# Kernel optimization log

Hardware: AMD Instinct MI355X
Metric: run time of the kernel (lower is better)

Reference implementation:

```python
import jax, jax.numpy as jnp
import numpy as np


def setup_inputs() -> dict:
    key = jax.random.key(0)
    ks = jax.random.split(key, 7)
    N, T, E = 4, 2048, 1024
    s = 1.0 / np.sqrt(E)
    return {
        "X": jax.random.normal(ks[0], (N, T, E), dtype=jnp.float32),
        "Wq": jax.random.normal(ks[1], (E, E), dtype=jnp.float32) * s,
        "bq": jax.random.normal(ks[2], (E,), dtype=jnp.float32) * 0.01,
        "Wk": jax.random.normal(ks[3], (E, E), dtype=jnp.float32) * s,
        "bk": jax.random.normal(ks[4], (E,), dtype=jnp.float32) * 0.01,
        "Wv": jax.random.normal(ks[5], (E, E), dtype=jnp.float32) * s,
        "bv": jax.random.normal(ks[6], (E,), dtype=jnp.float32) * 0.01,
    }


def reference(X, Wq, bq, Wk, bk, Wv, bv):
    # QKV projections: [N,T,E] @ [E,E] + [E]
    q = jnp.einsum("nte,ef->ntf", X, Wq) + bq
    k = jnp.einsum("nte,ef->ntf", X, Wk) + bk
    v = jnp.einsum("nte,ef->ntf", X, Wv) + bv
    # Unscaled full attention (module does NOT divide by sqrt(E))
    sim = jnp.einsum("nqe,nke->nqk", q, k)         # [N,T,T]
    weight = jax.nn.softmax(sim, axis=2)
    return jnp.einsum("nqk,nke->nqe", weight, v)    # [N,T,E]
```

## Files before the change

kernel.cpp:

```cpp
#include <hip/hip_runtime.h>

typedef unsigned short u16;
typedef unsigned int u32;
typedef float floatx4 __attribute__((ext_vector_type(4)));
typedef __bf16 bf16x8 __attribute__((ext_vector_type(8)));

__device__ __forceinline__ u16 bf16_rne(float x) {
  u32 u = __builtin_bit_cast(u32, x);
  return (u16)((u + 0x7FFFu + ((u >> 16) & 1u)) >> 16);
}
__device__ __forceinline__ float bf16f(u16 h) {
  u32 u = ((u32)h) << 16;
  return __builtin_bit_cast(float, u);
}
__device__ __forceinline__ void g2l16(const u16* g, u16* l) {
  __builtin_amdgcn_global_load_lds((const __attribute__((address_space(1))) u32*)g,
                                   (__attribute__((address_space(3))) u32*)l, 16, 0, 0);
}
__device__ __forceinline__ floatx4 mfma16(bf16x8 a, bf16x8 b, floatx4 c) {
  return __builtin_amdgcn_mfma_f32_16x16x32_bf16(a, b, c, 0, 0, 0);
}
#define SB() __builtin_amdgcn_sched_barrier(0)

__device__ __forceinline__ void xcd_swizzle(int& bx, int& by, int& bz) {
  const int gx = gridDim.x, gy = gridDim.y;
  int nb = gx * gy * gridDim.z;
  int flat = blockIdx.x + gx * (blockIdx.y + gy * blockIdx.z);
  int swz = flat;
  if ((nb & 7) == 0) {
    int cpx = nb >> 3;
    swz = (flat & 7) * cpx + (flat >> 3);
  }
  bz = swz / (gx * gy);
  int rem = swz - bz * gx * gy;
  by = rem / gx;
  bx = rem - by * gx;
}

__global__ void split_x_kernel(const float* __restrict__ X, u16* __restrict__ Xh,
                               u16* __restrict__ Xl, int n4) {
  int i = blockIdx.x * blockDim.x + threadIdx.x;
  int stride = gridDim.x * blockDim.x;
  for (; i < n4; i += stride) {
    float4 x = reinterpret_cast<const float4*>(X)[i];
    float v[4] = {x.x, x.y, x.z, x.w};
    u16 hh[4], ll[4];
#pragma unroll
    for (int j = 0; j < 4; ++j) {
      hh[j] = bf16_rne(v[j]);
      ll[j] = bf16_rne(v[j] - bf16f(hh[j]));
    }
    reinterpret_cast<ushort4*>(Xh)[i] = make_ushort4(hh[0], hh[1], hh[2], hh[3]);
    reinterpret_cast<ushort4*>(Xl)[i] = make_ushort4(ll[0], ll[1], ll[2], ll[3]);
  }
}

__global__ void wsplit_t_kernel(const float* __restrict__ W, u16* __restrict__ Th,
                                u16* __restrict__ Tl) {
  __shared__ float tile[32][33];
  int tx = threadIdx.x, ty = threadIdx.y;
  int f0 = blockIdx.x * 32, e0 = blockIdx.y * 32;
  tile[ty][tx] = W[(e0 + ty) * 1024 + f0 + tx];
  __syncthreads();
  float v = tile[tx][ty];
  u16 h = bf16_rne(v);
  Th[(f0 + ty) * 1024 + e0 + tx] = h;
  Tl[(f0 + ty) * 1024 + e0 + tx] = bf16_rne(v - bf16f(h));
}

template <int EPI>
__global__ __launch_bounds__(512, 2) void gemm8_split(
    const u16* __restrict__ Ah, const u16* __restrict__ Al,
    const u16* __restrict__ Bh, const u16* __restrict__ Bl,
    float* __restrict__ C, u16* __restrict__ Oh, u16* __restrict__ Ol,
    const float* __restrict__ b1, const float* __restrict__ b2, int NH,
    int N, int K, int lda, int ldb, long sA, long sB, long sC) {
  __shared__ u16 lds[2][4][256 * 32];
  const int tid = threadIdx.x;
  int bx, by, bz;
  xcd_swizzle(bx, by, bz);
  const int z = bz;
  const int brow = by * 256;
  const int bcol = bx * 256;
  const int w = tid >> 6, l = tid & 63;
  const int wm = w >> 2, wn = w & 3;
  const int fr = l & 15, kq = l >> 4;

  const u16* gA0 = Ah + (long)z * sA + (long)brow * lda;
  const u16* gA1 = Al + (long)z * sA + (long)brow * lda;
  const u16* gB0 = Bh + (long)z * sB + (long)bcol * ldb;
  const u16* gB1 = Bl + (long)z * sB + (long)bcol * ldb;

  const int r0 = tid >> 2, s0 = tid & 3;
  const int r1 = (tid + 512) >> 2, s1 = (tid + 512) & 3;
  const long aOff0 = (long)r0 * lda + ((s0 ^ ((r0 >> 1) & 3)) << 3);
  const long aOff1 = (long)r1 * lda + ((s1 ^ ((r1 >> 1) & 3)) << 3);
  const long bOff0 = (long)r0 * ldb + ((s0 ^ ((r0 >> 1) & 3)) << 3);
  const long bOff1 = (long)r1 * ldb + ((s1 ^ ((r1 >> 1) & 3)) << 3);
  const int d0 = tid * 8, d1 = (tid + 512) * 8;

  auto STAGE = [&](int b, int k0) {
    g2l16(gA0 + aOff0 + k0, &lds[b][0][d0]);
    g2l16(gA0 + aOff1 + k0, &lds[b][0][d1]);
    g2l16(gA1 + aOff0 + k0, &lds[b][1][d0]);
    g2l16(gA1 + aOff1 + k0, &lds[b][1][d1]);
    g2l16(gB0 + bOff0 + k0, &lds[b][2][d0]);
    g2l16(gB0 + bOff1 + k0, &lds[b][2][d1]);
    g2l16(gB1 + bOff0 + k0, &lds[b][3][d0]);
    g2l16(gB1 + bOff1 + k0, &lds[b][3][d1]);
  };

  int aoffs[8], boffs[4];
#pragma unroll
  for (int m = 0; m < 8; ++m) {
    int r = wm * 128 + m * 16 + fr;
    aoffs[m] = r * 32 + (((kq ^ (r >> 1)) & 3) << 3);
  }
#pragma unroll
  for (int n = 0; n < 4; ++n) {
    int r = wn * 64 + n * 16 + fr;
    boffs[n] = r * 32 + (((kq ^ (r >> 1)) & 3) << 3);
  }

  floatx4 acc[8][4];
#pragma unroll
  for (int m = 0; m < 8; ++m)
#pragma unroll
    for (int n = 0; n < 4; ++n)
#pragma unroll
      for (int j = 0; j < 4; ++j) acc[m][n][j] = 0.f;

  const int NT = K >> 5;
  STAGE(0, 0);
  STAGE(1, 32);
  SB();
  asm volatile("s_waitcnt vmcnt(8)" ::: "memory");
  SB(); __builtin_amdgcn_s_barrier(); SB();

  bf16x8 fa_h[4], fa_l[4], fb_h[4], fb_l[4];

  for (int t = 0; t < NT; ++t) {
    const int p = t & 1;
    const u16* LAh = &lds[p][0][0];
    const u16* LAl = &lds[p][1][0];
    const u16* LBh = &lds[p][2][0];
    const u16* LBl = &lds[p][3][0];

#pragma unroll
    for (int m = 0; m < 4; ++m) {
      fa_h[m] = *(const bf16x8*)(LAh + aoffs[m]);
      fa_l[m] = *(const bf16x8*)(LAl + aoffs[m]);
    }
#pragma unroll
    for (int n = 0; n < 2; ++n) {
      fb_h[n] = *(const bf16x8*)(LBh + boffs[n]);
      fb_l[n] = *(const bf16x8*)(LBl + boffs[n]);
    }
    SB(); __builtin_amdgcn_s_barrier();
    asm volatile("s_waitcnt lgkmcnt(0)" ::: "memory");
    SB();
    __builtin_amdgcn_s_setprio(1);
#pragma unroll
    for (int m = 0; m < 4; ++m)
#pragma unroll
      for (int n = 0; n < 2; ++n) acc[m][n] = mfma16(fa_h[m], fb_h[n], acc[m][n]);
#pragma unroll
    for (int m = 0; m < 4; ++m)
#pragma unroll
      for (int n = 0; n < 2; ++n) acc[m][n] = mfma16(fa_h[m], fb_l[n], acc[m][n]);
#pragma unroll
    for (int m = 0; m < 4; ++m)
#pragma unroll
      for (int n = 0; n < 2; ++n) acc[m][n] = mfma16(fa_l[m], fb_h[n], acc[m][n]);
    __builtin_amdgcn_s_setprio(0);
    SB(); __builtin_amdgcn_s_barrier(); SB();

#pragma unroll
    for (int n = 2; n < 4; ++n) {
      fb_h[n] = *(const bf16x8*)(LBh + boffs[n]);
      fb_l[n] = *(const bf16x8*)(LBl + boffs[n]);
    }
    SB(); __builtin_amdgcn_s_barrier();
    asm volatile("s_waitcnt lgkmcnt(0)" ::: "memory");
    SB();
    __builtin_amdgcn_s_setprio(1);
#pragma unroll
    for (int m = 0; m < 4; ++m)
#pragma unroll
      for (int n = 2; n < 4; ++n) acc[m][n] = mfma16(fa_h[m], fb_h[n], acc[m][n]);
#pragma unroll
    for (int m = 0; m < 4; ++m)
#pragma unroll
      for (int n = 2; n < 4; ++n) acc[m][n] = mfma16(fa_h[m], fb_l[n], acc[m][n]);
#pragma unroll
    for (int m = 0; m < 4; ++m)
#pragma unroll
      for (int n = 2; n < 4; ++n) acc[m][n] = mfma16(fa_l[m], fb_h[n], acc[m][n]);
    __builtin_amdgcn_s_setprio(0);
    SB(); __builtin_amdgcn_s_barrier(); SB();

#pragma unroll
    for (int m = 0; m < 4; ++m) {
      fa_h[m] = *(const bf16x8*)(LAh + aoffs[m + 4]);
      fa_l[m] = *(const bf16x8*)(LAl + aoffs[m + 4]);
    }
    SB(); __builtin_amdgcn_s_barrier();
    asm volatile("s_waitcnt lgkmcnt(0)" ::: "memory");
    SB();
    __builtin_amdgcn_s_setprio(1);
#pragma unroll
    for (int m = 0; m < 4; ++m)
#pragma unroll
      for (int n = 0; n < 2; ++n) acc[m + 4][n] = mfma16(fa_h[m], fb_h[n], acc[m + 4][n]);
#pragma unroll
    for (int m = 0; m < 4; ++m)
#pragma unroll
      for (int n = 0; n < 2; ++n) acc[m + 4][n] = mfma16(fa_h[m], fb_l[n], acc[m + 4][n]);
#pragma unroll
    for (int m = 0; m < 4; ++m)
#pragma unroll
      for (int n = 0; n < 2; ++n) acc[m + 4][n] = mfma16(fa_l[m], fb_h[n], acc[m + 4][n]);
    __builtin_amdgcn_s_setprio(0);
    SB(); __builtin_amdgcn_s_barrier(); SB();

    if (t + 2 < NT) STAGE(p, (t + 2) << 5);
    SB();
    __builtin_amdgcn_s_setprio(1);
#pragma unroll
    for (int m = 0; m < 4; ++m)
#pragma unroll
      for (int n = 2; n < 4; ++n) acc[m + 4][n] = mfma16(fa_h[m], fb_h[n], acc[m + 4][n]);
#pragma unroll
    for (int m = 0; m < 4; ++m)
#pragma unroll
      for (int n = 2; n < 4; ++n) acc[m + 4][n] = mfma16(fa_h[m], fb_l[n], acc[m + 4][n]);
#pragma unroll
    for (int m = 0; m < 4; ++m)
#pragma unroll
      for (int n = 2; n < 4; ++n) acc[m + 4][n] = mfma16(fa_l[m], fb_h[n], acc[m + 4][n]);
    __builtin_amdgcn_s_setprio(0);
    SB();
    if (t + 2 < NT) {
      asm volatile("s_waitcnt vmcnt(8)" ::: "memory");
    } else {
      asm volatile("s_waitcnt vmcnt(0)" ::: "memory");
    }
    SB(); __builtin_amdgcn_s_barrier(); SB();
  }

#pragma unroll
  for (int m = 0; m < 8; ++m)
#pragma unroll
    for (int n = 0; n < 4; ++n)
#pragma unroll
      for (int j = 0; j < 4; ++j) {
        int gr = brow + wm * 128 + m * 16 + kq * 4 + j;
        int gc = bcol + wn * 64 + n * 16 + fr;
        float v = acc[m][n][j];
        if (EPI == 0) {
          C[(long)z * sC + (long)gr * N + gc] = v;
        } else {
          v += (gc < NH) ? b1[gc] : b2[gc - NH];
          u16 h = bf16_rne(v);
          long idx = (long)gr * N + gc;
          Oh[idx] = h;
          Ol[idx] = bf16_rne(v - bf16f(h));
        }
      }
}

template <int EPI>
__global__ __launch_bounds__(512, 2) void gemm8_plain(
    const u16* __restrict__ A, const u16* __restrict__ B,
    float* __restrict__ C, u16* __restrict__ Oh, const float* __restrict__ bias,
    int N, int K, int lda, int ldb, long sA, long sB, long sC) {
  __shared__ u16 lds[2][24576];
  const int BOFF = 8192;
  const int tid = threadIdx.x;
  int bx, by, bz;
  xcd_swizzle(bx, by, bz);
  const int z = bz;
  const int brow = by * 128;
  const int bcol = bx * 256;
  const int w = tid >> 6, l = tid & 63;
  const int wm = (w >> 2) * 64, wn = (w & 3) * 64;
  const int fr = l & 15, kq = l >> 4;

  const u16* gA = A + (long)z * sA + (long)brow * lda;
  const u16* gB = B + (long)z * sB + (long)bcol * ldb;

  long aO[2], bO[4];
  int aD[2], bD[4];
#pragma unroll
  for (int i = 0; i < 2; ++i) {
    int c = tid + i * 512, r = c >> 3, s = c & 7;
    aO[i] = (long)r * lda + ((s ^ (r & 7)) << 3);
    aD[i] = c * 8;
  }
#pragma unroll
  for (int i = 0; i < 4; ++i) {
    int c = tid + i * 512, r = c >> 3, s = c & 7;
    bO[i] = (long)r * ldb + ((s ^ (r & 7)) << 3);
    bD[i] = BOFF + c * 8;
  }

  auto STAGE = [&](int b, int k0) {
#pragma unroll
    for (int i = 0; i < 2; ++i) g2l16(gA + aO[i] + k0, &lds[b][aD[i]]);
#pragma unroll
    for (int i = 0; i < 4; ++i) g2l16(gB + bO[i] + k0, &lds[b][bD[i]]);
  };

  int aoffs[4][2], boffs[4][2];
#pragma unroll
  for (int m = 0; m < 4; ++m) {
    int r = wm + m * 16 + fr;
#pragma unroll
    for (int k = 0; k < 2; ++k) aoffs[m][k] = r * 64 + ((((k * 4 + kq) ^ r) & 7) << 3);
  }
#pragma unroll
  for (int n = 0; n < 4; ++n) {
    int r = wn + n * 16 + fr;
#pragma unroll
    for (int k = 0; k < 2; ++k) boffs[n][k] = BOFF + r * 64 + ((((k * 4 + kq) ^ r) & 7) << 3);
  }

  floatx4 acc[4][4];
#pragma unroll
  for (int m = 0; m < 4; ++m)
#pragma unroll
    for (int n = 0; n < 4; ++n)
#pragma unroll
      for (int j = 0; j < 4; ++j) acc[m][n][j] = 0.f;

  const int NT = K >> 6;
  STAGE(0, 0);
  STAGE(1, 64);
  SB();
  asm volatile("s_waitcnt vmcnt(6)" ::: "memory");
  SB(); __builtin_amdgcn_s_barrier(); SB();

  bf16x8 fa[2][2], fb[4][2];

  for (int t = 0; t < NT; ++t) {
    const int p = t & 1;
    const u16* L = &lds[p][0];

#pragma unroll
    for (int m = 0; m < 2; ++m)
#pragma unroll
      for (int k = 0; k < 2; ++k) fa[m][k] = *(const bf16x8*)(L + aoffs[m][k]);
#pragma unroll
    for (int n = 0; n < 2; ++n)
#pragma unroll
      for (int k = 0; k < 2; ++k) fb[n][k] = *(const bf16x8*)(L + boffs[n][k]);
    SB(); __builtin_amdgcn_s_barrier();
    asm volatile("s_waitcnt lgkmcnt(0)" ::: "memory");
    SB();
    __builtin_amdgcn_s_setprio(1);
#pragma unroll
    for (int m = 0; m < 2; ++m)
#pragma unroll
      for (int n = 0; n < 2; ++n) acc[m][n] = mfma16(fa[m][0], fb[n][0], acc[m][n]);
#pragma unroll
    for (int m = 0; m < 2; ++m)
#pragma unroll
      for (int n = 0; n < 2; ++n) acc[m][n] = mfma16(fa[m][1], fb[n][1], acc[m][n]);
    __builtin_amdgcn_s_setprio(0);
    SB(); __builtin_amdgcn_s_barrier(); SB();

#pragma unroll
    for (int n = 2; n < 4; ++n)
#pragma unroll
      for (int k = 0; k < 2; ++k) fb[n][k] = *(const bf16x8*)(L + boffs[n][k]);
    SB(); __builtin_amdgcn_s_barrier();
    asm volatile("s_waitcnt lgkmcnt(0)" ::: "memory");
    SB();
    __builtin_amdgcn_s_setprio(1);
#pragma unroll
    for (int m = 0; m < 2; ++m)
#pragma unroll
      for (int n = 2; n < 4; ++n) acc[m][n] = mfma16(fa[m][0], fb[n][0], acc[m][n]);
#pragma unroll
    for (int m = 0; m < 2; ++m)
#pragma unroll
      for (int n = 2; n < 4; ++n) acc[m][n] = mfma16(fa[m][1], fb[n][1], acc[m][n]);
    __builtin_amdgcn_s_setprio(0);
    SB(); __builtin_amdgcn_s_barrier(); SB();

#pragma unroll
    for (int m = 0; m < 2; ++m)
#pragma unroll
      for (int k = 0; k < 2; ++k) fa[m][k] = *(const bf16x8*)(L + aoffs[m + 2][k]);
    SB(); __builtin_amdgcn_s_barrier();
    asm volatile("s_waitcnt lgkmcnt(0)" ::: "memory");
    SB();
    __builtin_amdgcn_s_setprio(1);
#pragma unroll
    for (int m = 0; m < 2; ++m)
#pragma unroll
      for (int n = 0; n < 2; ++n) acc[m + 2][n] = mfma16(fa[m][0], fb[n][0], acc[m + 2][n]);
#pragma unroll
    for (int m = 0; m < 2; ++m)
#pragma unroll
      for (int n = 0; n < 2; ++n) acc[m + 2][n] = mfma16(fa[m][1], fb[n][1], acc[m + 2][n]);
    __builtin_amdgcn_s_setprio(0);
    SB(); __builtin_amdgcn_s_barrier(); SB();

    if (t + 2 < NT) STAGE(p, (t + 2) << 6);
    SB();
    __builtin_amdgcn_s_setprio(1);
#pragma unroll
    for (int m = 0; m < 2; ++m)
#pragma unroll
      for (int n = 2; n < 4; ++n) acc[m + 2][n] = mfma16(fa[m][0], fb[n][0], acc[m + 2][n]);
#pragma unroll
    for (int m = 0; m < 2; ++m)
#pragma unroll
      for (int n = 2; n < 4; ++n) acc[m + 2][n] = mfma16(fa[m][1], fb[n][1], acc[m + 2][n]);
    __builtin_amdgcn_s_setprio(0);
    SB();
    if (t + 2 < NT) {
      asm volatile("s_waitcnt vmcnt(6)" ::: "memory");
    } else {
      asm volatile("s_waitcnt vmcnt(0)" ::: "memory");
    }
    SB(); __builtin_amdgcn_s_barrier(); SB();
  }

#pragma unroll
  for (int m = 0; m < 4; ++m)
#pragma unroll
    for (int n = 0; n < 4; ++n)
#pragma unroll
      for (int j = 0; j < 4; ++j) {
        int gr = brow + wm + m * 16 + kq * 4 + j;
        int gc = bcol + wn + n * 16 + fr;
        float v = acc[m][n][j];
        if (EPI == 0) {
          C[(long)z * sC + (long)gr * N + gc] = v;
        } else {
          v += bias[gc];
          long oi = ((long)((gr >> 11) * 1024 + gc)) * 2048 + (gr & 2047);
          Oh[oi] = bf16_rne(v);
        }
      }
}

__global__ __launch_bounds__(256) void softmax_kernel(const float* __restrict__ S,
                                                      u16* __restrict__ Wgt) {
  const long row = blockIdx.x;
  const float4* src = reinterpret_cast<const float4*>(S + row * 2048);
  const int t = threadIdx.x;
  float4 x0 = src[t];
  float4 x1 = src[t + 256];
  float m = fmaxf(fmaxf(fmaxf(x0.x, x0.y), fmaxf(x0.z, x0.w)),
                  fmaxf(fmaxf(x1.x, x1.y), fmaxf(x1.z, x1.w)));
#pragma unroll
  for (int s = 32; s > 0; s >>= 1) m = fmaxf(m, __shfl_xor(m, s));
  __shared__ float redm[4];
  __shared__ float reds[4];
  if ((t & 63) == 0) redm[t >> 6] = m;
  __syncthreads();
  m = fmaxf(fmaxf(redm[0], redm[1]), fmaxf(redm[2], redm[3]));
  float e[8];
  e[0] = __expf(x0.x - m); e[1] = __expf(x0.y - m);
  e[2] = __expf(x0.z - m); e[3] = __expf(x0.w - m);
  e[4] = __expf(x1.x - m); e[5] = __expf(x1.y - m);
  e[6] = __expf(x1.z - m); e[7] = __expf(x1.w - m);
  float s = ((e[0] + e[1]) + (e[2] + e[3])) + ((e[4] + e[5]) + (e[6] + e[7]));
#pragma unroll
  for (int k = 32; k > 0; k >>= 1) s += __shfl_xor(s, k);
  if ((t & 63) == 0) reds[t >> 6] = s;
  __syncthreads();
  s = (reds[0] + reds[1]) + (reds[2] + reds[3]);
  float inv = 1.f / s;
  u32* dst = reinterpret_cast<u32*>(Wgt + row * 2048);
  dst[2 * t] = (u32)bf16_rne(e[0] * inv) | ((u32)bf16_rne(e[1] * inv) << 16);
  dst[2 * t + 1] = (u32)bf16_rne(e[2] * inv) | ((u32)bf16_rne(e[3] * inv) << 16);
  dst[2 * (t + 256)] = (u32)bf16_rne(e[4] * inv) | ((u32)bf16_rne(e[5] * inv) << 16);
  dst[2 * (t + 256) + 1] = (u32)bf16_rne(e[6] * inv) | ((u32)bf16_rne(e[7] * inv) << 16);
}

extern "C" void kernel_launch(void* const* d_in, const int* in_sizes, int n_in,
                              void* d_out, int out_size, void* d_ws, size_t ws_size,
                              hipStream_t stream) {
  const float* X = (const float*)d_in[0];
  const float* Wq = (const float*)d_in[1];
  const float* bq = (const float*)d_in[2];
  const float* Wk = (const float*)d_in[3];
  const float* bk = (const float*)d_in[4];
  const float* Wv = (const float*)d_in[5];
  const float* bv = (const float*)d_in[6];
  float* out = (float*)d_out;

  char* ws = (char*)d_ws;
  const size_t MB = 1ull << 20;
  u16* Xh = (u16*)(ws + 0 * MB);
  u16* Xl = (u16*)(ws + 16 * MB);
  u16* Wqkh = (u16*)(ws + 32 * MB);
  u16* Wqkl = (u16*)(ws + 36 * MB);
  u16* Wvh = (u16*)(ws + 40 * MB);
  u16* Wvl = (u16*)(ws + 42 * MB);
  float* sim = (float*)(ws);
  u16* qkh = (u16*)(ws + 64 * MB);
  u16* qkl = (u16*)(ws + 96 * MB);
  u16* vt = (u16*)(ws + 128 * MB);
  u16* wb = (u16*)(ws + 64 * MB);

  split_x_kernel<<<4096, 256, 0, stream>>>(X, Xh, Xl, (8192 * 1024) / 4);
  wsplit_t_kernel<<<dim3(32, 32), dim3(32, 32), 0, stream>>>(Wq, Wqkh, Wqkl);
  wsplit_t_kernel<<<dim3(32, 32), dim3(32, 32), 0, stream>>>(Wk, Wqkh + 1024 * 1024,
                                                             Wqkl + 1024 * 1024);
  wsplit_t_kernel<<<dim3(32, 32), dim3(32, 32), 0, stream>>>(Wv, Wvh, Wvl);
  gemm8_split<1><<<dim3(8, 32, 1), 512, 0, stream>>>(
      Xh, Xl, Wqkh, Wqkl, nullptr, qkh, qkl, bq, bk, 1024,
      2048, 1024, 1024, 1024, 0, 0, 0);
  gemm8_plain<2><<<dim3(4, 64, 1), 512, 0, stream>>>(
      Xh, Wvh, nullptr, vt, bv, 1024, 1024, 1024, 1024, 0, 0, 0);
  gemm8_split<0><<<dim3(8, 8, 4), 512, 0, stream>>>(
      qkh, qkl, qkh + 1024, qkl + 1024, sim, nullptr, nullptr, nullptr, nullptr, 0,
      2048, 1024, 2048, 2048, 2048L * 2048, 2048L * 2048, 2048L * 2048);
  softmax_kernel<<<8192, 256, 0, stream>>>(sim, wb);
  gemm8_plain<0><<<dim3(4, 16, 4), 512, 0, stream>>>(
      wb, vt, out, nullptr, nullptr, 1024, 2048, 2048, 2048,
      2048L * 2048, 1024L * 2048, 2048L * 1024);
}
```

Measured before the change: 357.2 us.

## Switch GEMM kernels from 16x16x32 to 32x32x16 MFMA tiles

Replaces the 16x16x32 bf16 MFMA instruction with the 32x32x16 variant in both GEMM kernels. The LDS fragment offsets, accumulator layout and epilogue index mapping are reworked to match, and the per-iteration schedule shrinks from four sub-phases with barriers to two k-substeps. The larger MFMA tile needs fewer LDS fragment reads per FLOP and fewer barriers, at the cost of different register pressure and less interleaving of loads with compute.

```diff
diff --git a/kernel.cpp b/kernel.cpp
--- a/kernel.cpp
+++ b/kernel.cpp
@@ -2,7 +2,7 @@
 
 typedef unsigned short u16;
 typedef unsigned int u32;
-typedef float floatx4 __attribute__((ext_vector_type(4)));
+typedef float floatx16 __attribute__((ext_vector_type(16)));
 typedef __bf16 bf16x8 __attribute__((ext_vector_type(8)));
 
 __device__ __forceinline__ u16 bf16_rne(float x) {
@@ -17,8 +17,8 @@
   __builtin_amdgcn_global_load_lds((const __attribute__((address_space(1))) u32*)g,
                                    (__attribute__((address_space(3))) u32*)l, 16, 0, 0);
 }
-__device__ __forceinline__ floatx4 mfma16(bf16x8 a, bf16x8 b, floatx4 c) {
-  return __builtin_amdgcn_mfma_f32_16x16x32_bf16(a, b, c, 0, 0, 0);
+__device__ __forceinline__ floatx16 mfma32(bf16x8 a, bf16x8 b, floatx16 c) {
+  return __builtin_amdgcn_mfma_f32_32x32x16_bf16(a, b, c, 0, 0, 0);
 }
 #define SB() __builtin_amdgcn_sched_barrier(0)
 
@@ -84,7 +84,7 @@
   const int bcol = bx * 256;
   const int w = tid >> 6, l = tid & 63;
   const int wm = w >> 2, wn = w & 3;
-  const int fr = l & 15, kq = l >> 4;
+  const int lr = l & 31, lh = l >> 5;
 
   const u16* gA0 = Ah + (long)z * sA + (long)brow * lda;
   const u16* gA1 = Al + (long)z * sA + (long)brow * lda;
@@ -110,25 +110,29 @@
     g2l16(gB1 + bOff1 + k0, &lds[b][3][d1]);
   };
 
-  int aoffs[8], boffs[4];
-#pragma unroll
-  for (int m = 0; m < 8; ++m) {
-    int r = wm * 128 + m * 16 + fr;
-    aoffs[m] = r * 32 + (((kq ^ (r >> 1)) & 3) << 3);
-  }
-#pragma unroll
-  for (int n = 0; n < 4; ++n) {
-    int r = wn * 64 + n * 16 + fr;
-    boffs[n] = r * 32 + (((kq ^ (r >> 1)) & 3) << 3);
-  }
-
-  floatx4 acc[8][4];
-#pragma unroll
-  for (int m = 0; m < 8; ++m)
-#pragma unroll
-    for (int n = 0; n < 4; ++n)
-#pragma unroll
-      for (int j = 0; j < 4; ++j) acc[m][n][j] = 0.f;
+  int aoffs[4][2], boffs[2][2];
+#pragma unroll
+  for (int m = 0; m < 4; ++m) {
+    int r = wm * 128 + m * 32 + lr;
+#pragma unroll
+    for (int ks = 0; ks < 2; ++ks)
+      aoffs[m][ks] = r * 32 + ((((ks * 2 + lh) ^ ((r >> 1) & 3)) & 3) << 3);
+  }
+#pragma unroll
+  for (int n = 0; n < 2; ++n) {
+    int r = wn * 64 + n * 32 + lr;
+#pragma unroll
+    for (int ks = 0; ks < 2; ++ks)
+      boffs[n][ks] = r * 32 + ((((ks * 2 + lh) ^ ((r >> 1) & 3)) & 3) << 3);
+  }
+
+  floatx16 acc[4][2];
+#pragma unroll
+  for (int m = 0; m < 4; ++m)
+#pragma unroll
+    for (int n = 0; n < 2; ++n)
+#pragma unroll
+      for (int j = 0; j < 16; ++j) acc[m][n][j] = 0.f;
 
   const int NT = K >> 5;
   STAGE(0, 0);
@@ -137,7 +141,7 @@
   asm volatile("s_waitcnt vmcnt(8)" ::: "memory");
   SB(); __builtin_amdgcn_s_barrier(); SB();
 
-  bf16x8 fa_h[4], fa_l[4], fb_h[4], fb_l[4];
+  bf16x8 fah[4], fal[4], fbh[2], fbl[2];
 
   for (int t = 0; t < NT; ++t) {
     const int p = t & 1;
@@ -148,13 +152,13 @@
 
 #pragma unroll
     for (int m = 0; m < 4; ++m) {
-      fa_h[m] = *(const bf16x8*)(LAh + aoffs[m]);
-      fa_l[m] = *(const bf16x8*)(LAl + aoffs[m]);
+      fah[m] = *(const bf16x8*)(LAh + aoffs[m][0]);
+      fal[m] = *(const bf16x8*)(LAl + aoffs[m][0]);
     }
 #pragma unroll
     for (int n = 0; n < 2; ++n) {
-      fb_h[n] = *(const bf16x8*)(LBh + boffs[n]);
-      fb_l[n] = *(const bf16x8*)(LBl + boffs[n]);
+      fbh[n] = *(const bf16x8*)(LBh + boffs[n][0]);
+      fbl[n] = *(const bf16x8*)(LBl + boffs[n][0]);
     }
     SB(); __builtin_amdgcn_s_barrier();
     asm volatile("s_waitcnt lgkmcnt(0)" ::: "memory");
@@ -163,81 +167,46 @@
 #pragma unroll
     for (int m = 0; m < 4; ++m)
 #pragma unroll
-      for (int n = 0; n < 2; ++n) acc[m][n] = mfma16(fa_h[m], fb_h[n], acc[m][n]);
-#pragma unroll
-    for (int m = 0; m < 4; ++m)
-#pragma unroll
-      for (int n = 0; n < 2; ++n) acc[m][n] = mfma16(fa_h[m], fb_l[n], acc[m][n]);
-#pragma unroll
-    for (int m = 0; m < 4; ++m)
-#pragma unroll
-      for (int n = 0; n < 2; ++n) acc[m][n] = mfma16(fa_l[m], fb_h[n], acc[m][n]);
+      for (int n = 0; n < 2; ++n) acc[m][n] = mfma32(fah[m], fbh[n], acc[m][n]);
+#pragma unroll
+    for (int m = 0; m < 4; ++m)
+#pragma unroll
+      for (int n = 0; n < 2; ++n) acc[m][n] = mfma32(fah[m], fbl[n], acc[m][n]);
+#pragma unroll
+    for (int m = 0; m < 4; ++m)
+#pragma unroll
+      for (int n = 0; n < 2; ++n) acc[m][n] = mfma32(fal[m], fbh[n], acc[m][n]);
     __builtin_amdgcn_s_setprio(0);
     SB(); __builtin_amdgcn_s_barrier(); SB();
 
 #pragma unroll
-    for (int n = 2; n < 4; ++n) {
-      fb_h[n] = *(const bf16x8*)(LBh + boffs[n]);
-      fb_l[n] = *(const bf16x8*)(LBl + boffs[n]);
-    }
-    SB(); __builtin_amdgcn_s_barrier();
+    for (int m = 0; m < 4; ++m) {
+      fah[m] = *(const bf16x8*)(LAh + aoffs[m][1]);
+      fal[m] = *(const bf16x8*)(LAl + aoffs[m][1]);
+    }
+#pragma unroll
+    for (int n = 0; n < 2; ++n) {
+      fbh[n] = *(const bf16x8*)(LBh + boffs[n][1]);
+      fbl[n] = *(const bf16x8*)(LBl + boffs[n][1]);
+    }
+    SB();
     asm volatile("s_waitcnt lgkmcnt(0)" ::: "memory");
+    SB(); __builtin_amdgcn_s_barrier(); SB();
+    if (t + 2 < NT) STAGE(p, (t + 2) << 5);
     SB();
     __builtin_amdgcn_s_setprio(1);
 #pragma unroll
     for (int m = 0; m < 4; ++m)
 #pragma unroll
-      for (int n = 2; n < 4; ++n) acc[m][n] = mfma16(fa_h[m], fb_h[n], acc[m][n]);
-#pragma unroll
-    for (int m = 0; m < 4; ++m)
-#pragma unroll
-      for (int n = 2; n < 4; ++n) acc[m][n] = mfma16(fa_h[m], fb_l[n], acc[m][n]);
-#pragma unroll
-    for (int m = 0; m < 4; ++m)
-#pragma unroll
-      for (int n = 2; n < 4; ++n) acc[m][n] = mfma16(fa_l[m], fb_h[n], acc[m][n]);
-    __builtin_amdgcn_s_setprio(0);
-    SB(); __builtin_amdgcn_s_barrier(); SB();
-
-#pragma unroll
-    for (int m = 0; m < 4; ++m) {
-      fa_h[m] = *(const bf16x8*)(LAh + aoffs[m + 4]);
-      fa_l[m] = *(const bf16x8*)(LAl + aoffs[m + 4]);
-    }
-    SB(); __builtin_amdgcn_s_barrier();
-    asm volatile("s_waitcnt lgkmcnt(0)" ::: "memory");
-    SB();
-    __builtin_amdgcn_s_setprio(1);
-#pragma unroll
-    for (int m = 0; m < 4; ++m)
-#pragma unroll
-      for (int n = 0; n < 2; ++n) acc[m + 4][n] = mfma16(fa_h[m], fb_h[n], acc[m + 4][n]);
-#pragma unroll
-    for (int m = 0; m < 4; ++m)
-#pragma unroll
-      for (int n = 0; n < 2; ++n) acc[m + 4][n] = mfma16(fa_h[m], fb_l[n], acc[m + 4][n]);
-#pragma unroll
-    for (int m = 0; m < 4; ++m)
-#pragma unroll
-      for (int n = 0; n < 2; ++n) acc[m + 4][n] = mfma16(fa_l[m], fb_h[n], acc[m + 4][n]);
-    __builtin_amdgcn_s_setprio(0);
-    SB(); __builtin_amdgcn_s_barrier(); SB();
-
-    if (t + 2 < NT) STAGE(p, (t + 2) << 5);
-    SB();
-    __builtin_amdgcn_s_setprio(1);
-#pragma unroll
-    for (int m = 0; m < 4; ++m)
-#pragma unroll
-      for (int n = 2; n < 4; ++n) acc[m + 4][n] = mfma16(fa_h[m], fb_h[n], acc[m + 4][n]);
-#pragma unroll
-    for (int m = 0; m < 4; ++m)
-#pragma unroll
-      for (int n = 2; n < 4; ++n) acc[m + 4][n] = mfma16(fa_h[m], fb_l[n], acc[m + 4][n]);
-#pragma unroll
-    for (int m = 0; m < 4; ++m)
-#pragma unroll
-      for (int n = 2; n < 4; ++n) acc[m + 4][n] = mfma16(fa_l[m], fb_h[n], acc[m + 4][n]);
+      for (int n = 0; n < 2; ++n) acc[m][n] = mfma32(fah[m], fbh[n], acc[m][n]);
+#pragma unroll
+    for (int m = 0; m < 4; ++m)
+#pragma unroll
+      for (int n = 0; n < 2; ++n) acc[m][n] = mfma32(fah[m], fbl[n], acc[m][n]);
+#pragma unroll
+    for (int m = 0; m < 4; ++m)
+#pragma unroll
+      for (int n = 0; n < 2; ++n) acc[m][n] = mfma32(fal[m], fbh[n], acc[m][n]);
     __builtin_amdgcn_s_setprio(0);
     SB();
     if (t + 2 < NT) {
@@ -249,14 +218,14 @@
   }
 
 #pragma unroll
-  for (int m = 0; m < 8; ++m)
-#pragma unroll
-    for (int n = 0; n < 4; ++n)
-#pragma unroll
-      for (int j = 0; j < 4; ++j) {
-        int gr = brow + wm * 128 + m * 16 + kq * 4 + j;
-        int gc = bcol + wn * 64 + n * 16 + fr;
-        float v = acc[m][n][j];
+  for (int m = 0; m < 4; ++m)
+#pragma unroll
+    for (int n = 0; n < 2; ++n)
+#pragma unroll
+      for (int reg = 0; reg < 16; ++reg) {
+        int gr = brow + wm * 128 + m * 32 + (reg & 3) + 8 * (reg >> 2) + 4 * lh;
+        int gc = bcol + wn * 64 + n * 32 + lr;
+        float v = acc[m][n][reg];
         if (EPI == 0) {
           C[(long)z * sC + (long)gr * N + gc] = v;
         } else {
@@ -283,8 +252,8 @@
   const int brow = by * 128;
   const int bcol = bx * 256;
   const int w = tid >> 6, l = tid & 63;
-  const int wm = (w >> 2) * 64, wn = (w & 3) * 64;
-  const int fr = l & 15, kq = l >> 4;
+  const int wm = w >> 2, wn = w & 3;
+  const int lr = l & 31, lh = l >> 5;
 
   const u16* gA = A + (long)z * sA + (long)brow * lda;
   const u16* gB = B + (long)z * sB + (long)bcol * ldb;
@@ -311,27 +280,29 @@
     for (int i = 0; i < 4; ++i) g2l16(gB + bO[i] + k0, &lds[b][bD[i]]);
   };
 
-  int aoffs[4][2], boffs[4][2];
-#pragma unroll
-  for (int m = 0; m < 4; ++m) {
-    int r = wm + m * 16 + fr;
-#pragma unroll
-    for (int k = 0; k < 2; ++k) aoffs[m][k] = r * 64 + ((((k * 4 + kq) ^ r) & 7) << 3);
-  }
-#pragma unroll
-  for (int n = 0; n < 4; ++n) {
-    int r = wn + n * 16 + fr;
-#pragma unroll
-    for (int k = 0; k < 2; ++k) boffs[n][k] = BOFF + r * 64 + ((((k * 4 + kq) ^ r) & 7) << 3);
-  }
-
-  floatx4 acc[4][4];
-#pragma unroll
-  for (int m = 0; m < 4; ++m)
-#pragma unroll
-    for (int n = 0; n < 4; ++n)
-#pragma unroll
-      for (int j = 0; j < 4; ++j) acc[m][n][j] = 0.f;
+  int aoffs[2][4], boffs[2][4];
+#pragma unroll
+  for (int m = 0; m < 2; ++m) {
+    int r = wm * 64 + m * 32 + lr;
+#pragma unroll
+    for (int ks = 0; ks < 4; ++ks)
+      aoffs[m][ks] = r * 64 + ((((ks * 2 + lh) ^ r) & 7) << 3);
+  }
+#pragma unroll
+  for (int n = 0; n < 2; ++n) {
+    int r = wn * 64 + n * 32 + lr;
+#pragma unroll
+    for (int ks = 0; ks < 4; ++ks)
+      boffs[n][ks] = BOFF + r * 64 + ((((ks * 2 + lh) ^ r) & 7) << 3);
+  }
+
+  floatx16 acc[2][2];
+#pragma unroll
+  for (int m = 0; m < 2; ++m)
+#pragma unroll
+    for (int n = 0; n < 2; ++n)
+#pragma unroll
+      for (int j = 0; j < 16; ++j) acc[m][n][j] = 0.f;
 
   const int NT = K >> 6;
   STAGE(0, 0);
@@ -340,7 +311,7 @@
   asm volatile("s_waitcnt vmcnt(6)" ::: "memory");
   SB(); __builtin_amdgcn_s_barrier(); SB();
 
-  bf16x8 fa[2][2], fb[4][2];
+  bf16x8 fa[2][2], fb[2][2];
 
   for (int t = 0; t < NT; ++t) {
     const int p = t & 1;
@@ -361,63 +332,36 @@
 #pragma unroll
     for (int m = 0; m < 2; ++m)
 #pragma unroll
-      for (int n = 0; n < 2; ++n) acc[m][n] = mfma16(fa[m][0], fb[n][0], acc[m][n]);
-#pragma unroll
-    for (int m = 0; m < 2; ++m)
-#pragma unroll
-      for (int n = 0; n < 2; ++n) acc[m][n] = mfma16(fa[m][1], fb[n][1], acc[m][n]);
+      for (int n = 0; n < 2; ++n) acc[m][n] = mfma32(fa[m][0], fb[n][0], acc[m][n]);
+#pragma unroll
+    for (int m = 0; m < 2; ++m)
+#pragma unroll
+      for (int n = 0; n < 2; ++n) acc[m][n] = mfma32(fa[m][1], fb[n][1], acc[m][n]);
     __builtin_amdgcn_s_setprio(0);
     SB(); __builtin_amdgcn_s_barrier(); SB();
 
 #pragma unroll
-    for (int n = 2; n < 4; ++n)
-#pragma unroll
-      for (int k = 0; k < 2; ++k) fb[n][k] = *(const bf16x8*)(L + boffs[n][k]);
-    SB(); __builtin_amdgcn_s_barrier();
+    for (int m = 0; m < 2; ++m)
+#pragma unroll
+      for (int k = 0; k < 2; ++k) fa[m][k] = *(const bf16x8*)(L + aoffs[m][k + 2]);
+#pragma unroll
+    for (int n = 0; n < 2; ++n)
+#pragma unroll
+      for (int k = 0; k < 2; ++k) fb[n][k] = *(const bf16x8*)(L + boffs[n][k + 2]);
+    SB();
     asm volatile("s_waitcnt lgkmcnt(0)" ::: "memory");
+    SB(); __builtin_amdgcn_s_barrier(); SB();
+    if (t + 2 < NT) STAGE(p, (t + 2) << 6);
     SB();
     __builtin_amdgcn_s_setprio(1);
 #pragma unroll
     for (int m = 0; m < 2; ++m)
 #pragma unroll
-      for (int n = 2; n < 4; ++n) acc[m][n] = mfma16(fa[m][0], fb[n][0], acc[m][n]);
-#pragma unroll
-    for (int m = 0; m < 2; ++m)
-#pragma unroll
-      for (int n = 2; n < 4; ++n) acc[m][n] = mfma16(fa[m][1], fb[n][1], acc[m][n]);
-    __builtin_amdgcn_s_setprio(0);
-    SB(); __builtin_amdgcn_s_barrier(); SB();
-
-#pragma unroll
-    for (int m = 0; m < 2; ++m)
-#pragma unroll
-      for (int k = 0; k < 2; ++k) fa[m][k] = *(const bf16x8*)(L + aoffs[m + 2][k]);
-    SB(); __builtin_amdgcn_s_barrier();
-    asm volatile("s_waitcnt lgkmcnt(0)" ::: "memory");
-    SB();
-    __builtin_amdgcn_s_setprio(1);
-#pragma unroll
-    for (int m = 0; m < 2; ++m)
-#pragma unroll
-      for (int n = 0; n < 2; ++n) acc[m + 2][n] = mfma16(fa[m][0], fb[n][0], acc[m + 2][n]);
-#pragma unroll
-    for (int m = 0; m < 2; ++m)
-#pragma unroll
-      for (int n = 0; n < 2; ++n) acc[m + 2][n] = mfma16(fa[m][1], fb[n][1], acc[m + 2][n]);
-    __builtin_amdgcn_s_setprio(0);
-    SB(); __builtin_amdgcn_s_barrier(); SB();
-
-    if (t + 2 < NT) STAGE(p, (t + 2) << 6);
-    SB();
-    __builtin_amdgcn_s_setprio(1);
-#pragma unroll
-    for (int m = 0; m < 2; ++m)
-#pragma unroll
-      for (int n = 2; n < 4; ++n) acc[m + 2][n] = mfma16(fa[m][0], fb[n][0], acc[m + 2][n]);
-#pragma unroll
-    for (int m = 0; m < 2; ++m)
-#pragma unroll
-      for (int n = 2; n < 4; ++n) acc[m + 2][n] = mfma16(fa[m][1], fb[n][1], acc[m + 2][n]);
+      for (int n = 0; n < 2; ++n) acc[m][n] = mfma32(fa[m][0], fb[n][0], acc[m][n]);
+#pragma unroll
+    for (int m = 0; m < 2; ++m)
+#pragma unroll
+      for (int n = 0; n < 2; ++n) acc[m][n] = mfma32(fa[m][1], fb[n][1], acc[m][n]);
     __builtin_amdgcn_s_setprio(0);
     SB();
     if (t + 2 < NT) {
@@ -429,14 +373,14 @@
   }
 
 #pragma unroll
-  for (int m = 0; m < 4; ++m)
-#pragma unroll
-    for (int n = 0; n < 4; ++n)
-#pragma unroll
-      for (int j = 0; j < 4; ++j) {
-        int gr = brow + wm + m * 16 + kq * 4 + j;
-        int gc = bcol + wn + n * 16 + fr;
-        float v = acc[m][n][j];
+  for (int m = 0; m < 2; ++m)
+#pragma unroll
+    for (int n = 0; n < 2; ++n)
+#pragma unroll
+      for (int reg = 0; reg < 16; ++reg) {
+        int gr = brow + wm * 64 + m * 32 + (reg & 3) + 8 * (reg >> 2) + 4 * lh;
+        int gc = bcol + wn * 64 + n * 32 + lr;
+        float v = acc[m][n][reg];
         if (EPI == 0) {
           C[(long)z * sC + (long)gr * N + gc] = v;
         } else {
```

Result: slower. 393.2 us (+10.1%).
